# Performance work log

Hardware: AMD Instinct MI355X
Metric: run time of the kernel (lower is better)

Reference implementation:

```python
import jax, jax.numpy as jnp
import numpy as np

D_MODEL = 1024
HEADS = 16
DK = D_MODEL // HEADS
LAYERS = 4
BATCH = 8
SEQ = 1024
EPS = 1e-5


def _ln2(x):
    # torch LayerNorm([seq_len, d_model]) with default (untrained) affine: gamma=1, beta=0
    m = jnp.mean(x, axis=(1, 2), keepdims=True)
    v = jnp.var(x, axis=(1, 2), keepdims=True)
    return (x - m) * jax.lax.rsqrt(v + EPS)


def _pos_enc(seq_len, d_model):
    pos = jnp.arange(seq_len, dtype=jnp.float32)[:, None]
    i = jnp.arange(d_model)
    angle = pos / jnp.power(1000.0, (2 * (i // 2)).astype(jnp.float32) / d_model)
    return jnp.where(i % 2 == 0, jnp.sin(angle), jnp.cos(angle))  # [S, D]


def setup_inputs() -> dict:
    key = jax.random.key(0)
    ks = jax.random.split(key, 12)
    s = 0.02
    X = jax.random.normal(ks[0], (BATCH, SEQ, D_MODEL), dtype=jnp.float32)
    Wq = jax.random.normal(ks[1], (LAYERS, HEADS, DK, D_MODEL), dtype=jnp.float32) * s
    Wk = jax.random.normal(ks[2], (LAYERS, HEADS, DK, D_MODEL), dtype=jnp.float32) * s
    Wv = jax.random.normal(ks[3], (LAYERS, HEADS, DK, D_MODEL), dtype=jnp.float32) * s
    W0 = jax.random.normal(ks[4], (LAYERS, D_MODEL, D_MODEL), dtype=jnp.float32) * s
    Wr_w = jax.random.normal(ks[5], (LAYERS, D_MODEL, D_MODEL), dtype=jnp.float32) * s
    Wr_b = jax.random.normal(ks[6], (LAYERS, D_MODEL), dtype=jnp.float32) * s
    Wf0_w = jax.random.normal(ks[7], (LAYERS, D_MODEL, D_MODEL), dtype=jnp.float32) * s
    Wf0_b = jax.random.normal(ks[8], (LAYERS, D_MODEL), dtype=jnp.float32) * s
    Wf1_w = jax.random.normal(ks[9], (LAYERS, D_MODEL, D_MODEL), dtype=jnp.float32) * s
    Wf1_b = jax.random.normal(ks[10], (LAYERS, D_MODEL), dtype=jnp.float32) * s
    return {"X": X, "Wq": Wq, "Wk": Wk, "Wv": Wv, "W0": W0,
            "Wr_w": Wr_w, "Wr_b": Wr_b, "Wf0_w": Wf0_w, "Wf0_b": Wf0_b,
            "Wf1_w": Wf1_w, "Wf1_b": Wf1_b}


def reference(X, Wq, Wk, Wv, W0, Wr_w, Wr_b, Wf0_w, Wf0_b, Wf1_w, Wf1_b):
    B, S, D = X.shape
    x = X + _pos_enc(S, D)[None]
    scale = 1.0 / jnp.sqrt(jnp.float32(DK))
    for l in range(LAYERS):
        # batched multi-head projections (equivalent to per-head Linear + concat)
        Q = jnp.einsum('bsd,hkd->bhsk', x, Wq[l])
        K = jnp.einsum('bsd,hkd->bhsk', x, Wk[l])
        V = jnp.einsum('bsd,hkd->bhsk', x, Wv[l])
        scores = jnp.einsum('bhsk,bhtk->bhst', Q, K) * scale
        A = jax.nn.softmax(scores, axis=-1)
        O = jnp.einsum('bhst,bhtk->bhsk', A, V)
        O = O.transpose(0, 2, 1, 3).reshape(B, S, D)  # concat heads on feature dim
        mha = O @ W0[l].T
        r0 = _ln2(x + mha) @ Wr_w[l].T + Wr_b[l]
        ff = jax.nn.relu(r0 @ Wf0_w[l].T + Wf0_b[l]) @ Wf1_w[l].T + Wf1_b[l]
        x = _ln2(ff + r0) @ Wr_w[l].T + Wr_b[l]
    return x
```

## Files before the change

kernel.cpp:

```cpp
#include <hip/hip_runtime.h>
#include <hip/hip_bf16.h>
#include <math.h>

#define D_MODEL 1024
#define HEADS   16
#define DKV     64
#define LAYERS  4
#define BATCH   8
#define SEQ     1024
#define NTOK    (BATCH*SEQ)
#define LN_N    (SEQ*D_MODEL)
#define EPSV    1e-5f

typedef __attribute__((ext_vector_type(8))) short short8;
typedef __attribute__((ext_vector_type(4))) float floatx4;

__device__ __forceinline__ float bf2f(ushort u) {
    union { uint i; float f; } v; v.i = ((uint)u) << 16; return v.f;
}
__device__ __forceinline__ ushort f2bf(float f) {
    union { float f; uint i; } v; v.f = f;
    uint r = (v.i + 0x7fffu + ((v.i >> 16) & 1u)) >> 16;
    return (ushort)r;
}
__device__ __forceinline__ uint cvtpk(float a, float b) {
    uint r;
    asm("v_cvt_pk_bf16_f32 %0, %1, %2" : "=v"(r) : "v"(a), "v"(b));
    return r;
}
__device__ __forceinline__ void pl32(uint &a, uint &c) {
    asm volatile("v_permlane32_swap_b32 %0, %1" : "+v"(a), "+v"(c));
}
__device__ __forceinline__ void pl16(uint &a, uint &c) {
    asm volatile("v_permlane16_swap_b32 %0, %1" : "+v"(a), "+v"(c));
}

__device__ __forceinline__ void gload16(const ushort* g, ushort* l) {
    __builtin_amdgcn_global_load_lds(
        (const __attribute__((address_space(1))) void*)g,
        (__attribute__((address_space(3))) void*)l, 16, 0, 0);
}

#define TBUF (128*32)
__device__ __forceinline__ void gemm_core128(
    const ushort* __restrict__ A, const ushort* __restrict__ B,
    int lda, int ldb, int Kd,
    ushort* ldsA, ushort* ldsB, floatx4 (&acc)[4][4])
{
    const int tid  = threadIdx.x;
    const int lane = tid & 63;
    const int w    = tid >> 6;
    const int wm   = w >> 1, wn = w & 1;
    const int mn   = lane & 15, quad = lane >> 4;
    const int srow = tid >> 2;
    const int scol = (tid & 3) * 8;
    const ushort* ga = A + (size_t)srow * lda + scol;
    const ushort* gb = B + (size_t)srow * ldb + scol;
    ushort* la = ldsA + srow * 32 + scol;
    ushort* lb = ldsB + srow * 32 + scol;

    gload16(ga, la);
    gload16(ga + (size_t)64 * lda, la + 64 * 32);
    gload16(gb, lb);
    gload16(gb + (size_t)64 * ldb, lb + 64 * 32);
    __syncthreads();

    int cur = 0;
    for (int k0 = 0; k0 < Kd; k0 += 32) {
        const int nxt = cur ^ 1;
        if (k0 + 32 < Kd) {
            gload16(ga + k0 + 32, la + nxt * TBUF);
            gload16(ga + (size_t)64 * lda + k0 + 32, la + nxt * TBUF + 64 * 32);
            gload16(gb + k0 + 32, lb + nxt * TBUF);
            gload16(gb + (size_t)64 * ldb + k0 + 32, lb + nxt * TBUF + 64 * 32);
        }
        const ushort* cA = ldsA + cur * TBUF;
        const ushort* cB = ldsB + cur * TBUF;
        short8 af[4], bfr[4];
#pragma unroll
        for (int i = 0; i < 4; i++)
            af[i] = *(const short8*)(cA + (wm * 64 + i * 16 + mn) * 32 + quad * 8);
#pragma unroll
        for (int j = 0; j < 4; j++)
            bfr[j] = *(const short8*)(cB + (wn * 64 + j * 16 + mn) * 32 + quad * 8);
#pragma unroll
        for (int i = 0; i < 4; i++)
#pragma unroll
            for (int j = 0; j < 4; j++)
                acc[i][j] = __builtin_amdgcn_mfma_f32_16x16x32_bf16(af[i], bfr[j], acc[i][j], 0, 0, 0);
        __syncthreads();
        cur = nxt;
    }
}

__global__ __launch_bounds__(256) void gemm_bt128(
    const ushort* __restrict__ A, const ushort* __restrict__ B,
    const float* __restrict__ bias, ushort* __restrict__ C,
    const ushort* __restrict__ resid, float* __restrict__ stats,
    float* __restrict__ outF, int relu)
{
    __shared__ ushort ldsA[2 * TBUF], ldsB[2 * TBUF];
    __shared__ float sred1[4], sred2[4];
    const int lid = blockIdx.y * 64 + blockIdx.x;
    const int xcd = lid & 7, idx = lid >> 3;
    const int bx = xcd * 8 + (idx >> 3);
    const int by = idx & 7;
    floatx4 acc[4][4];
#pragma unroll
    for (int i = 0; i < 4; i++)
#pragma unroll
        for (int j = 0; j < 4; j++) acc[i][j] = (floatx4){0.f, 0.f, 0.f, 0.f};

    gemm_core128(A + (size_t)bx * 128 * D_MODEL,
                 B + (size_t)by * 128 * D_MODEL,
                 D_MODEL, D_MODEL, D_MODEL, ldsA, ldsB, acc);

    const int lane = threadIdx.x & 63, w = threadIdx.x >> 6;
    const int wm = w >> 1, wn = w & 1;
    const int mn = lane & 15, quad = lane >> 4;
    float ssum = 0.f, ssq = 0.f;
#pragma unroll
    for (int i = 0; i < 4; i++) {
#pragma unroll
        for (int j = 0; j < 4; j++) {
            int col = by * 128 + wn * 64 + j * 16 + mn;
            float bv = bias ? bias[col] : 0.f;
#pragma unroll
            for (int r = 0; r < 4; r++) {
                int row = bx * 128 + wm * 64 + i * 16 + quad * 4 + r;
                float v = acc[i][j][r] + bv;
                if (relu) v = fmaxf(v, 0.f);
                if (resid) {
                    v += bf2f(resid[(size_t)row * D_MODEL + col]);
                    ssum += v; ssq += v * v;
                }
                if (outF) outF[(size_t)row * D_MODEL + col] = v;
                else      C[(size_t)row * D_MODEL + col] = f2bf(v);
            }
        }
    }
    if (stats) {
        for (int o = 1; o < 64; o <<= 1) {
            ssum += __shfl_xor(ssum, o); ssq += __shfl_xor(ssq, o);
        }
        if (lane == 0) { sred1[w] = ssum; sred2[w] = ssq; }
        __syncthreads();
        if (threadIdx.x == 0) {
            int b = bx >> 3;
            atomicAdd(&stats[b * 32],      sred1[0] + sred1[1] + sred1[2] + sred1[3]);
            atomicAdd(&stats[b * 32 + 16], sred2[0] + sred2[1] + sred2[2] + sred2[3]);
        }
    }
}

__global__ __launch_bounds__(256) void gemm_qkv(
    const ushort* __restrict__ X, const ushort* __restrict__ Wq,
    const ushort* __restrict__ Wk, const ushort* __restrict__ Wv,
    ushort* __restrict__ Q, ushort* __restrict__ K, ushort* __restrict__ Vt)
{
    __shared__ ushort ldsA[2 * TBUF], ldsB[2 * TBUF];
    const int lid = blockIdx.y * 64 + blockIdx.x;
    const int xcd = lid & 7, idx = lid >> 3;
    const int bx = xcd * 8 + idx / 24;
    const int byy = idx % 24;
    const int which = byy >> 3;
    const int nb = byy & 7;
    const ushort* B = (which == 0) ? Wq : (which == 1) ? Wk : Wv;
    floatx4 acc[4][4];
#pragma unroll
    for (int i = 0; i < 4; i++)
#pragma unroll
        for (int j = 0; j < 4; j++) acc[i][j] = (floatx4){0.f, 0.f, 0.f, 0.f};

    gemm_core128(X + (size_t)bx * 128 * D_MODEL,
                 B + (size_t)nb * 128 * D_MODEL,
                 D_MODEL, D_MODEL, D_MODEL, ldsA, ldsB, acc);

    const int lane = threadIdx.x & 63, w = threadIdx.x >> 6;
    const int wm = w >> 1, wn = w & 1;
    const int mn = lane & 15, quad = lane >> 4;
    if (which == 2) {
#pragma unroll
        for (int i = 0; i < 4; i++) {
#pragma unroll
            for (int j = 0; j < 4; j++) {
                int col = nb * 128 + wn * 64 + j * 16 + mn;
                int h = col >> 6, kk = col & 63;
                int row0 = bx * 128 + wm * 64 + i * 16 + quad * 4;
                int b = row0 >> 10, t0 = row0 & 1023;
                uint2 uu;
                uu.x = cvtpk(acc[i][j][0], acc[i][j][1]);
                uu.y = cvtpk(acc[i][j][2], acc[i][j][3]);
                *(uint2*)(Vt + (((size_t)(b * HEADS + h)) * DKV + kk) * SEQ + t0) = uu;
            }
        }
    } else {
        ushort* dst = (which == 0) ? Q : K;
        const float scl = (which == 0) ? 0.125f : 1.0f;
#pragma unroll
        for (int i = 0; i < 4; i++) {
#pragma unroll
            for (int j = 0; j < 4; j++) {
                int col = nb * 128 + wn * 64 + j * 16 + mn;
#pragma unroll
                for (int r = 0; r < 4; r++) {
                    int row = bx * 128 + wm * 64 + i * 16 + quad * 4 + r;
                    dst[(size_t)row * D_MODEL + col] = f2bf(acc[i][j][r] * scl);
                }
            }
        }
    }
}

__global__ __launch_bounds__(256) void flash_attn(
    const ushort* __restrict__ Q, const ushort* __restrict__ K,
    const ushort* __restrict__ Vt, ushort* __restrict__ O)
{
    __shared__ ushort lK[64 * 128];
    __shared__ ushort lV[64 * 128];
    const int tid = threadIdx.x, lane = tid & 63, w = tid >> 6;
    const int mn = lane & 15, quad = lane >> 4;
    const int pair = blockIdx.x;
    const int qt = blockIdx.y;
    const int b = pair >> 4, h = pair & 15;
    const ushort* Qb = Q + ((size_t)b * SEQ) * D_MODEL + h * DKV;
    const ushort* Kb = K + ((size_t)b * SEQ) * D_MODEL + h * DKV;
    const ushort* Vb = Vt + (size_t)pair * DKV * SEQ;

    short8 bq[2][2];
#pragma unroll
    for (int i = 0; i < 2; i++)
#pragma unroll
        for (int kk = 0; kk < 2; kk++)
            bq[i][kk] = *(const short8*)(Qb +
                (size_t)(qt * 128 + w * 32 + i * 16 + mn) * D_MODEL + kk * 32 + quad * 8);

    auto stage_K = [&](int tkk) {
#pragma unroll
        for (int c = 0; c < 4; c++) {
            int lin = c * 256 + tid;
            int rw = lin >> 4;
            int cc0 = (lin & 15) ^ (rw & 7);
            int r = rw + ((cc0 >> 3) << 6);
            gload16(Kb + (size_t)(tkk * 128 + r) * D_MODEL + (cc0 & 7) * 8,
                    lK + lin * 8);
        }
    };
    auto stage_V = [&](int tkk) {
#pragma unroll
        for (int c = 0; c < 4; c++) {
            int lin = c * 256 + tid;
            int rw = lin >> 4;
            int cc0 = (lin & 15) ^ (rw & 7);
            gload16(Vb + (size_t)rw * SEQ + tkk * 128 + cc0 * 8,
                    lV + lin * 8);
        }
    };

    stage_K(0); stage_V(0);
    __syncthreads();

    floatx4 acc_o[2][4];
    float lrow[2] = {0.f, 0.f};
#pragma unroll
    for (int i = 0; i < 2; i++)
#pragma unroll
        for (int jo = 0; jo < 4; jo++) acc_o[i][jo] = (floatx4){0.f, 0.f, 0.f, 0.f};

    for (int tk = 0; tk < 8; tk++) {
        floatx4 s[2][8];
#pragma unroll
        for (int i = 0; i < 2; i++)
#pragma unroll
            for (int j = 0; j < 8; j++) s[i][j] = (floatx4){0.f, 0.f, 0.f, 0.f};
        __builtin_amdgcn_s_setprio(1);
#pragma unroll
        for (int kk = 0; kk < 2; kk++) {
#pragma unroll
            for (int j = 0; j < 8; j++) {
                int krow = (j & 3) * 16 + mn;
                int kch = (((j >> 2) * 8 + kk * 4 + quad) ^ (mn & 7));
                short8 ak = *(const short8*)(lK + krow * 128 + kch * 8);
                s[0][j] = __builtin_amdgcn_mfma_f32_16x16x32_bf16(ak, bq[0][kk], s[0][j], 0, 0, 0);
                s[1][j] = __builtin_amdgcn_mfma_f32_16x16x32_bf16(ak, bq[1][kk], s[1][j], 0, 0, 0);
            }
        }
        __builtin_amdgcn_s_setprio(0);
        __syncthreads();
        if (tk < 7) stage_K(tk + 1);

        uint pw[2][8][2];
#pragma unroll
        for (int i = 0; i < 2; i++) {
            float ps = 0.f;
#pragma unroll
            for (int j = 0; j < 8; j++) {
                float p0 = __expf(s[i][j][0]), p1 = __expf(s[i][j][1]);
                float p2 = __expf(s[i][j][2]), p3 = __expf(s[i][j][3]);
                ps += (p0 + p1) + (p2 + p3);
                pw[i][j][0] = cvtpk(p0, p1);
                pw[i][j][1] = cvtpk(p2, p3);
            }
            ps += __shfl_xor(ps, 16);
            ps += __shfl_xor(ps, 32);
            lrow[i] += ps;
        }

        __builtin_amdgcn_s_setprio(1);
#pragma unroll
        for (int kk = 0; kk < 4; kk++) {
            union { short8 s8; uint u[4]; } pa[2];
#pragma unroll
            for (int i = 0; i < 2; i++) {
                uint A = pw[i][2 * kk][0],     Bw = pw[i][2 * kk][1];
                uint C = pw[i][2 * kk + 1][0], D  = pw[i][2 * kk + 1][1];
                pl32(A, C);  pl16(A, C);
                pl32(Bw, D); pl16(Bw, D);
                pa[i].u[0] = A; pa[i].u[1] = Bw; pa[i].u[2] = C; pa[i].u[3] = D;
            }
#pragma unroll
            for (int jo = 0; jo < 4; jo++) {
                int vch = ((kk * 4 + quad) ^ (mn & 7));
                short8 bv = *(const short8*)(lV + (jo * 16 + mn) * 128 + vch * 8);
                acc_o[0][jo] = __builtin_amdgcn_mfma_f32_16x16x32_bf16(pa[0].s8, bv, acc_o[0][jo], 0, 0, 0);
                acc_o[1][jo] = __builtin_amdgcn_mfma_f32_16x16x32_bf16(pa[1].s8, bv, acc_o[1][jo], 0, 0, 0);
            }
        }
        __builtin_amdgcn_s_setprio(0);
        __syncthreads();
        if (tk < 7) stage_V(tk + 1);
    }

#pragma unroll
    for (int i = 0; i < 2; i++)
#pragma unroll
        for (int r = 0; r < 4; r++) {
            float rs = __shfl(lrow[i], quad * 4 + r);
            float rinv = 1.f / rs;
            int row = qt * 128 + w * 32 + i * 16 + quad * 4 + r;
#pragma unroll
            for (int jo = 0; jo < 4; jo++)
                O[((size_t)b * SEQ + row) * D_MODEL + h * DKV + jo * 16 + mn] =
                    f2bf(acc_o[i][jo][r] * rinv);
        }
}

__global__ __launch_bounds__(256) void cvt_f32_bf16(const float* __restrict__ src,
                                                    ushort* __restrict__ dst) {
    size_t base = ((size_t)blockIdx.x * 256 + threadIdx.x) * 8;
    float4 a = *(const float4*)(src + base);
    float4 b = *(const float4*)(src + base + 4);
    short8 o;
    o[0] = (short)f2bf(a.x); o[1] = (short)f2bf(a.y);
    o[2] = (short)f2bf(a.z); o[3] = (short)f2bf(a.w);
    o[4] = (short)f2bf(b.x); o[5] = (short)f2bf(b.y);
    o[6] = (short)f2bf(b.z); o[7] = (short)f2bf(b.w);
    *(short8*)(dst + base) = o;
}

__global__ __launch_bounds__(256) void add_pos(const float* __restrict__ X,
                                               ushort* __restrict__ x) {
    size_t idx = (size_t)blockIdx.x * 256 + threadIdx.x;
    int d = (int)(idx & (D_MODEL - 1));
    int s = (int)((idx >> 10) & (SEQ - 1));
    float freq = powf(1000.f, (float)(2 * (d >> 1)) * (1.f / (float)D_MODEL));
    float ang = (float)s / freq;
    float pe = (d & 1) ? cosf(ang) : sinf(ang);
    x[idx] = f2bf(X[idx] + pe);
}

__global__ __launch_bounds__(256) void ln_apply(
    const ushort* __restrict__ S, ushort* __restrict__ Y,
    const float* __restrict__ stats)
{
    size_t base = ((size_t)blockIdx.x * 256 + threadIdx.x) * 8;
    int b = blockIdx.x >> 9;
    float mean = stats[b * 32] * (1.f / (float)LN_N);
    float var = stats[b * 32 + 16] * (1.f / (float)LN_N) - mean * mean;
    float r = rsqrtf(var + EPSV);
    short8 sv = *(const short8*)(S + base);
    short8 ov;
#pragma unroll
    for (int i = 0; i < 8; i++) ov[i] = (short)f2bf((bf2f((ushort)sv[i]) - mean) * r);
    *(short8*)(Y + base) = ov;
}

__global__ void zero_stats(float* stats) { stats[threadIdx.x] = 0.f; }

extern "C" void kernel_launch(void* const* d_in, const int* in_sizes, int n_in,
                              void* d_out, int out_size, void* d_ws, size_t ws_size,
                              hipStream_t stream) {
    const float* X    = (const float*)d_in[0];
    const float* Wq   = (const float*)d_in[1];
    const float* Wk   = (const float*)d_in[2];
    const float* Wv   = (const float*)d_in[3];
    const float* W0   = (const float*)d_in[4];
    const float* Wr_w = (const float*)d_in[5];
    const float* Wr_b = (const float*)d_in[6];
    const float* Wf0w = (const float*)d_in[7];
    const float* Wf0b = (const float*)d_in[8];
    const float* Wf1w = (const float*)d_in[9];
    const float* Wf1b = (const float*)d_in[10];
    float* out = (float*)d_out;

    char* ws = (char*)d_ws;
    size_t off = 0;
    auto alloc = [&](size_t bytes) -> void* {
        void* p = ws + off; off += (bytes + 255) & ~(size_t)255; return p;
    };
    const size_t ACT = (size_t)NTOK * D_MODEL * sizeof(ushort);
    const size_t WTE = (size_t)LAYERS * D_MODEL * D_MODEL;
    ushort* x  = (ushort*)alloc(ACT);
    ushort* bQ = (ushort*)alloc(ACT);
    ushort* bK = (ushort*)alloc(ACT);
    ushort* bV = (ushort*)alloc(ACT);
    ushort* bO = (ushort*)alloc(ACT);
    ushort* wq  = (ushort*)alloc(WTE * 2);
    ushort* wk  = (ushort*)alloc(WTE * 2);
    ushort* wv  = (ushort*)alloc(WTE * 2);
    ushort* w0  = (ushort*)alloc(WTE * 2);
    ushort* wr  = (ushort*)alloc(WTE * 2);
    ushort* wf0 = (ushort*)alloc(WTE * 2);
    ushort* wf1 = (ushort*)alloc(WTE * 2);
    float* stats = (float*)alloc(256 * sizeof(float));

    const int EW_BLOCKS = (NTOK * D_MODEL) / (256 * 8);
    const int CVT_BLOCKS = (int)(WTE / (256 * 8));
    const dim3 GEMM_GRID(NTOK / 128, D_MODEL / 128);
    const dim3 QKV_GRID(NTOK / 128, 3 * D_MODEL / 128);
    const dim3 FLASH_GRID(BATCH * HEADS, SEQ / 128);

    cvt_f32_bf16<<<CVT_BLOCKS, 256, 0, stream>>>(Wq,   wq);
    cvt_f32_bf16<<<CVT_BLOCKS, 256, 0, stream>>>(Wk,   wk);
    cvt_f32_bf16<<<CVT_BLOCKS, 256, 0, stream>>>(Wv,   wv);
    cvt_f32_bf16<<<CVT_BLOCKS, 256, 0, stream>>>(W0,   w0);
    cvt_f32_bf16<<<CVT_BLOCKS, 256, 0, stream>>>(Wr_w, wr);
    cvt_f32_bf16<<<CVT_BLOCKS, 256, 0, stream>>>(Wf0w, wf0);
    cvt_f32_bf16<<<CVT_BLOCKS, 256, 0, stream>>>(Wf1w, wf1);

    add_pos<<<(NTOK * D_MODEL) / 256, 256, 0, stream>>>(X, x);

    for (int l = 0; l < LAYERS; l++) {
        const size_t WO = (size_t)l * D_MODEL * D_MODEL;
        const ushort* Wq_l  = wq  + WO;
        const ushort* Wk_l  = wk  + WO;
        const ushort* Wv_l  = wv  + WO;
        const ushort* W0_l  = w0  + WO;
        const ushort* Wr_l  = wr  + WO;
        const ushort* W0w_l = wf0 + WO;
        const ushort* W1w_l = wf1 + WO;
        const float* Wrb_l = Wr_b + (size_t)l * D_MODEL;
        const float* W0b_l = Wf0b + (size_t)l * D_MODEL;
        const float* W1b_l = Wf1b + (size_t)l * D_MODEL;

        gemm_qkv<<<QKV_GRID, 256, 0, stream>>>(x, Wq_l, Wk_l, Wv_l, bQ, bK, bV);

        flash_attn<<<FLASH_GRID, 256, 0, stream>>>(bQ, bK, bV, bO);

        zero_stats<<<1, 256, 0, stream>>>(stats);
        gemm_bt128<<<GEMM_GRID, 256, 0, stream>>>(bO, W0_l, nullptr, bK,
            x, stats, nullptr, 0);
        ln_apply<<<EW_BLOCKS, 256, 0, stream>>>(bK, bO, stats);
        gemm_bt128<<<GEMM_GRID, 256, 0, stream>>>(bO, Wr_l, Wrb_l, bV,
            nullptr, nullptr, nullptr, 0);
        gemm_bt128<<<GEMM_GRID, 256, 0, stream>>>(bV, W0w_l, W0b_l, bQ,
            nullptr, nullptr, nullptr, 1);
        zero_stats<<<1, 256, 0, stream>>>(stats);
        gemm_bt128<<<GEMM_GRID, 256, 0, stream>>>(bQ, W1w_l, W1b_l, bK,
            bV, stats, nullptr, 0);
        ln_apply<<<EW_BLOCKS, 256, 0, stream>>>(bK, bO, stats);
        gemm_bt128<<<GEMM_GRID, 256, 0, stream>>>(bO, Wr_l, Wrb_l, x,
            nullptr, nullptr, (l == LAYERS - 1) ? out : nullptr, 0);
    }
}
```

Measured before the change: 1.501 ms.

## Fold LayerNorm into following GEMM epilogue via weight column sums; swizzle LDS with BK=64

Removes the standalone ln_apply passes. The following Wr GEMM runs on the un-normalized activations, and its epilogue applies (acc - mean*colsum(W)) * rstd using precomputed per-row sums of the bf16 weights and per-sample stats. The GEMM core is templated on K-tile size with an XOR-swizzled LDS layout, and the main GEMMs use BK=64 to halve barriers per K. Per-layer stats buffers are zeroed once up front instead of by separate launches. This trades extra LDS and possible cancellation error in the mean subtraction for fewer kernels and less activation traffic.

```diff
diff --git a/kernel.cpp b/kernel.cpp
--- a/kernel.cpp
+++ b/kernel.cpp
@@ -41,65 +41,74 @@
         (__attribute__((address_space(3))) void*)l, 16, 0, 0);
 }
 
-#define TBUF (128*32)
-__device__ __forceinline__ void gemm_core128(
+template<int BK>
+__device__ __forceinline__ void gemm_coreT(
     const ushort* __restrict__ A, const ushort* __restrict__ B,
     int lda, int ldb, int Kd,
     ushort* ldsA, ushort* ldsB, floatx4 (&acc)[4][4])
 {
+    constexpr int CH = BK / 8;
+    constexpr int TB = 128 * BK;
     const int tid  = threadIdx.x;
     const int lane = tid & 63;
     const int w    = tid >> 6;
     const int wm   = w >> 1, wn = w & 1;
     const int mn   = lane & 15, quad = lane >> 4;
-    const int srow = tid >> 2;
-    const int scol = (tid & 3) * 8;
-    const ushort* ga = A + (size_t)srow * lda + scol;
-    const ushort* gb = B + (size_t)srow * ldb + scol;
-    ushort* la = ldsA + srow * 32 + scol;
-    ushort* lb = ldsB + srow * 32 + scol;
-
-    gload16(ga, la);
-    gload16(ga + (size_t)64 * lda, la + 64 * 32);
-    gload16(gb, lb);
-    gload16(gb + (size_t)64 * ldb, lb + 64 * 32);
+
+    auto stage = [&](int k0, int buf) {
+#pragma unroll
+        for (int s = 0; s < CH / 2; s++) {
+            int lin = s * 256 + tid;
+            int r   = lin / CH;
+            int cp  = lin % CH;
+            int cs_ = cp ^ (r & (CH - 1));
+            gload16(A + (size_t)r * lda + k0 + cs_ * 8, ldsA + buf * TB + lin * 8);
+            gload16(B + (size_t)r * ldb + k0 + cs_ * 8, ldsB + buf * TB + lin * 8);
+        }
+    };
+
+    stage(0, 0);
     __syncthreads();
 
     int cur = 0;
-    for (int k0 = 0; k0 < Kd; k0 += 32) {
-        const int nxt = cur ^ 1;
-        if (k0 + 32 < Kd) {
-            gload16(ga + k0 + 32, la + nxt * TBUF);
-            gload16(ga + (size_t)64 * lda + k0 + 32, la + nxt * TBUF + 64 * 32);
-            gload16(gb + k0 + 32, lb + nxt * TBUF);
-            gload16(gb + (size_t)64 * ldb + k0 + 32, lb + nxt * TBUF + 64 * 32);
-        }
-        const ushort* cA = ldsA + cur * TBUF;
-        const ushort* cB = ldsB + cur * TBUF;
-        short8 af[4], bfr[4];
-#pragma unroll
-        for (int i = 0; i < 4; i++)
-            af[i] = *(const short8*)(cA + (wm * 64 + i * 16 + mn) * 32 + quad * 8);
-#pragma unroll
-        for (int j = 0; j < 4; j++)
-            bfr[j] = *(const short8*)(cB + (wn * 64 + j * 16 + mn) * 32 + quad * 8);
-#pragma unroll
-        for (int i = 0; i < 4; i++)
-#pragma unroll
-            for (int j = 0; j < 4; j++)
-                acc[i][j] = __builtin_amdgcn_mfma_f32_16x16x32_bf16(af[i], bfr[j], acc[i][j], 0, 0, 0);
+    for (int k0 = 0; k0 < Kd; k0 += BK) {
+        if (k0 + BK < Kd) stage(k0 + BK, cur ^ 1);
+        const ushort* cA = ldsA + cur * TB;
+        const ushort* cB = ldsB + cur * TB;
+#pragma unroll
+        for (int kk = 0; kk < BK / 32; kk++) {
+            short8 af[4], bfr[4];
+#pragma unroll
+            for (int i = 0; i < 4; i++) {
+                int r = wm * 64 + i * 16 + mn;
+                int c = (kk * 4 + quad) ^ (r & (CH - 1));
+                af[i] = *(const short8*)(cA + r * BK + c * 8);
+            }
+#pragma unroll
+            for (int j = 0; j < 4; j++) {
+                int r = wn * 64 + j * 16 + mn;
+                int c = (kk * 4 + quad) ^ (r & (CH - 1));
+                bfr[j] = *(const short8*)(cB + r * BK + c * 8);
+            }
+#pragma unroll
+            for (int i = 0; i < 4; i++)
+#pragma unroll
+                for (int j = 0; j < 4; j++)
+                    acc[i][j] = __builtin_amdgcn_mfma_f32_16x16x32_bf16(af[i], bfr[j], acc[i][j], 0, 0, 0);
+        }
         __syncthreads();
-        cur = nxt;
+        cur ^= 1;
     }
 }
 
 __global__ __launch_bounds__(256) void gemm_bt128(
     const ushort* __restrict__ A, const ushort* __restrict__ B,
     const float* __restrict__ bias, ushort* __restrict__ C,
-    const ushort* __restrict__ resid, float* __restrict__ stats,
-    float* __restrict__ outF, int relu)
+    const ushort* __restrict__ resid, float* __restrict__ statsOut,
+    float* __restrict__ outF, int relu,
+    const float* __restrict__ lnIn, const float* __restrict__ csum)
 {
-    __shared__ ushort ldsA[2 * TBUF], ldsB[2 * TBUF];
+    __shared__ ushort ldsA[2 * 128 * 64], ldsB[2 * 128 * 64];
     __shared__ float sred1[4], sred2[4];
     const int lid = blockIdx.y * 64 + blockIdx.x;
     const int xcd = lid & 7, idx = lid >> 3;
@@ -111,13 +120,20 @@
 #pragma unroll
         for (int j = 0; j < 4; j++) acc[i][j] = (floatx4){0.f, 0.f, 0.f, 0.f};
 
-    gemm_core128(A + (size_t)bx * 128 * D_MODEL,
-                 B + (size_t)by * 128 * D_MODEL,
-                 D_MODEL, D_MODEL, D_MODEL, ldsA, ldsB, acc);
+    gemm_coreT<64>(A + (size_t)bx * 128 * D_MODEL,
+                   B + (size_t)by * 128 * D_MODEL,
+                   D_MODEL, D_MODEL, D_MODEL, ldsA, ldsB, acc);
 
     const int lane = threadIdx.x & 63, w = threadIdx.x >> 6;
     const int wm = w >> 1, wn = w & 1;
     const int mn = lane & 15, quad = lane >> 4;
+    const int bsmp = bx >> 3;
+    float mean = 0.f, rln = 1.f;
+    if (lnIn) {
+        float sum = lnIn[bsmp], sq = lnIn[32 + bsmp];
+        mean = sum * (1.f / (float)LN_N);
+        rln  = rsqrtf(sq * (1.f / (float)LN_N) - mean * mean + EPSV);
+    }
     float ssum = 0.f, ssq = 0.f;
 #pragma unroll
     for (int i = 0; i < 4; i++) {
@@ -125,10 +141,13 @@
         for (int j = 0; j < 4; j++) {
             int col = by * 128 + wn * 64 + j * 16 + mn;
             float bv = bias ? bias[col] : 0.f;
+            float cj = csum ? csum[col] : 0.f;
 #pragma unroll
             for (int r = 0; r < 4; r++) {
                 int row = bx * 128 + wm * 64 + i * 16 + quad * 4 + r;
-                float v = acc[i][j][r] + bv;
+                float v = acc[i][j][r];
+                if (lnIn) v = (v - mean * cj) * rln;
+                v += bv;
                 if (relu) v = fmaxf(v, 0.f);
                 if (resid) {
                     v += bf2f(resid[(size_t)row * D_MODEL + col]);
@@ -139,16 +158,15 @@
             }
         }
     }
-    if (stats) {
+    if (statsOut) {
         for (int o = 1; o < 64; o <<= 1) {
             ssum += __shfl_xor(ssum, o); ssq += __shfl_xor(ssq, o);
         }
         if (lane == 0) { sred1[w] = ssum; sred2[w] = ssq; }
         __syncthreads();
         if (threadIdx.x == 0) {
-            int b = bx >> 3;
-            atomicAdd(&stats[b * 32],      sred1[0] + sred1[1] + sred1[2] + sred1[3]);
-            atomicAdd(&stats[b * 32 + 16], sred2[0] + sred2[1] + sred2[2] + sred2[3]);
+            atomicAdd(&statsOut[bsmp],      sred1[0] + sred1[1] + sred1[2] + sred1[3]);
+            atomicAdd(&statsOut[32 + bsmp], sred2[0] + sred2[1] + sred2[2] + sred2[3]);
         }
     }
 }
@@ -158,7 +176,7 @@
     const ushort* __restrict__ Wk, const ushort* __restrict__ Wv,
     ushort* __restrict__ Q, ushort* __restrict__ K, ushort* __restrict__ Vt)
 {
-    __shared__ ushort ldsA[2 * TBUF], ldsB[2 * TBUF];
+    __shared__ ushort ldsA[2 * 128 * 32], ldsB[2 * 128 * 32];
     const int lid = blockIdx.y * 64 + blockIdx.x;
     const int xcd = lid & 7, idx = lid >> 3;
     const int bx = xcd * 8 + idx / 24;
@@ -172,9 +190,9 @@
 #pragma unroll
         for (int j = 0; j < 4; j++) acc[i][j] = (floatx4){0.f, 0.f, 0.f, 0.f};
 
-    gemm_core128(X + (size_t)bx * 128 * D_MODEL,
-                 B + (size_t)nb * 128 * D_MODEL,
-                 D_MODEL, D_MODEL, D_MODEL, ldsA, ldsB, acc);
+    gemm_coreT<32>(X + (size_t)bx * 128 * D_MODEL,
+                   B + (size_t)nb * 128 * D_MODEL,
+                   D_MODEL, D_MODEL, D_MODEL, ldsA, ldsB, acc);
 
     const int lane = threadIdx.x & 63, w = threadIdx.x >> 6;
     const int wm = w >> 1, wn = w & 1;
@@ -369,23 +387,26 @@
     x[idx] = f2bf(X[idx] + pe);
 }
 
-__global__ __launch_bounds__(256) void ln_apply(
-    const ushort* __restrict__ S, ushort* __restrict__ Y,
-    const float* __restrict__ stats)
-{
-    size_t base = ((size_t)blockIdx.x * 256 + threadIdx.x) * 8;
-    int b = blockIdx.x >> 9;
-    float mean = stats[b * 32] * (1.f / (float)LN_N);
-    float var = stats[b * 32 + 16] * (1.f / (float)LN_N) - mean * mean;
-    float r = rsqrtf(var + EPSV);
-    short8 sv = *(const short8*)(S + base);
-    short8 ov;
-#pragma unroll
-    for (int i = 0; i < 8; i++) ov[i] = (short)f2bf((bf2f((ushort)sv[i]) - mean) * r);
-    *(short8*)(Y + base) = ov;
-}
-
-__global__ void zero_stats(float* stats) { stats[threadIdx.x] = 0.f; }
+__global__ __launch_bounds__(256) void colsum_k(const ushort* __restrict__ W,
+                                                float* __restrict__ cs) {
+    int row = blockIdx.x * 4 + (threadIdx.x >> 6);
+    int lane = threadIdx.x & 63;
+    const ushort* Wr = W + (size_t)row * D_MODEL;
+    float s = 0.f;
+#pragma unroll
+    for (int p = 0; p < 2; p++) {
+        short8 v = *(const short8*)(Wr + p * 512 + lane * 8);
+#pragma unroll
+        for (int e = 0; e < 8; e++) s += bf2f((ushort)v[e]);
+    }
+#pragma unroll
+    for (int o = 1; o < 64; o <<= 1) s += __shfl_xor(s, o);
+    if (lane == 0) cs[row] = s;
+}
+
+__global__ void zero_stats512(float* stats) {
+    stats[threadIdx.x] = 0.f; stats[256 + threadIdx.x] = 0.f;
+}
 
 extern "C" void kernel_launch(void* const* d_in, const int* in_sizes, int n_in,
                               void* d_out, int out_size, void* d_ws, size_t ws_size,
@@ -422,9 +443,9 @@
     ushort* wr  = (ushort*)alloc(WTE * 2);
     ushort* wf0 = (ushort*)alloc(WTE * 2);
     ushort* wf1 = (ushort*)alloc(WTE * 2);
-    float* stats = (float*)alloc(256 * sizeof(float));
-
-    const int EW_BLOCKS = (NTOK * D_MODEL) / (256 * 8);
+    float* stats = (float*)alloc(8 * 64 * sizeof(float));
+    float* csr   = (float*)alloc(WTE / D_MODEL * sizeof(float));
+
     const int CVT_BLOCKS = (int)(WTE / (256 * 8));
     const dim3 GEMM_GRID(NTOK / 128, D_MODEL / 128);
     const dim3 QKV_GRID(NTOK / 128, 3 * D_MODEL / 128);
@@ -437,6 +458,8 @@
     cvt_f32_bf16<<<CVT_BLOCKS, 256, 0, stream>>>(Wr_w, wr);
     cvt_f32_bf16<<<CVT_BLOCKS, 256, 0, stream>>>(Wf0w, wf0);
     cvt_f32_bf16<<<CVT_BLOCKS, 256, 0, stream>>>(Wf1w, wf1);
+    colsum_k<<<LAYERS * D_MODEL / 4, 256, 0, stream>>>(wr, csr);
+    zero_stats512<<<1, 256, 0, stream>>>(stats);
 
     add_pos<<<(NTOK * D_MODEL) / 256, 256, 0, stream>>>(X, x);
 
@@ -452,24 +475,23 @@
         const float* Wrb_l = Wr_b + (size_t)l * D_MODEL;
         const float* W0b_l = Wf0b + (size_t)l * D_MODEL;
         const float* W1b_l = Wf1b + (size_t)l * D_MODEL;
+        const float* cs_l  = csr + (size_t)l * D_MODEL;
+        float* st0 = stats + (size_t)(2 * l) * 64;
+        float* st1 = stats + (size_t)(2 * l + 1) * 64;
 
         gemm_qkv<<<QKV_GRID, 256, 0, stream>>>(x, Wq_l, Wk_l, Wv_l, bQ, bK, bV);
 
         flash_attn<<<FLASH_GRID, 256, 0, stream>>>(bQ, bK, bV, bO);
 
-        zero_stats<<<1, 256, 0, stream>>>(stats);
         gemm_bt128<<<GEMM_GRID, 256, 0, stream>>>(bO, W0_l, nullptr, bK,
-            x, stats, nullptr, 0);
-        ln_apply<<<EW_BLOCKS, 256, 0, stream>>>(bK, bO, stats);
-        gemm_bt128<<<GEMM_GRID, 256, 0, stream>>>(bO, Wr_l, Wrb_l, bV,
-            nullptr, nullptr, nullptr, 0);
+            x, st0, nullptr, 0, nullptr, nullptr);
+        gemm_bt128<<<GEMM_GRID, 256, 0, stream>>>(bK, Wr_l, Wrb_l, bV,
+            nullptr, nullptr, nullptr, 0, st0, cs_l);
         gemm_bt128<<<GEMM_GRID, 256, 0, stream>>>(bV, W0w_l, W0b_l, bQ,
-            nullptr, nullptr, nullptr, 1);
-        zero_stats<<<1, 256, 0, stream>>>(stats);
-        gemm_bt128<<<GEMM_GRID, 256, 0, stream>>>(bQ, W1w_l, W1b_l, bK,
-            bV, stats, nullptr, 0);
-        ln_apply<<<EW_BLOCKS, 256, 0, stream>>>(bK, bO, stats);
+            nullptr, nullptr, nullptr, 1, nullptr, nullptr);
+        gemm_bt128<<<GEMM_GRID, 256, 0, stream>>>(bQ, W1w_l, W1b_l, bO,
+            bV, st1, nullptr, 0, nullptr, nullptr);
         gemm_bt128<<<GEMM_GRID, 256, 0, stream>>>(bO, Wr_l, Wrb_l, x,
-            nullptr, nullptr, (l == LAYERS - 1) ? out : nullptr, 0);
-    }
-}
+            nullptr, nullptr, (l == LAYERS - 1) ? out : nullptr, 0, st1, cs_l);
+    }
+}
```

Result: faster. 1.335 ms (-11.1%).
